# Kernel optimization log

Measured on AMD Instinct MI355X. Metric: run time of the kernel, lower is better.

The kernel has to match this reference:

```python
import jax, jax.numpy as jnp
import numpy as np

N_NODES = 50000
N_EDGES = 800000


def gcn_layer(x, edge_index, W, b):
    """PyG-style GCNConv: add self-loops, symmetric deg^-1/2 normalization,
    linear transform, scatter-sum aggregation at target nodes, plus bias."""
    n = x.shape[0]
    loops = jnp.arange(n)
    src = jnp.concatenate([edge_index[0], loops])  # [E+N]
    dst = jnp.concatenate([edge_index[1], loops])  # [E+N]
    deg = jax.ops.segment_sum(jnp.ones(src.shape, dtype=x.dtype), dst, num_segments=n)
    dinv = jnp.where(deg > 0, jax.lax.rsqrt(deg), jnp.zeros((), x.dtype))
    norm = dinv[src] * dinv[dst]               # [E+N]
    h = x @ W                                   # [N, out]
    msg = norm[:, None] * h[src]                # [E+N, out] gather
    out = jax.ops.segment_sum(msg, dst, num_segments=n)  # scatter-add
    return out + b


def setup_inputs() -> dict:
    key = jax.random.key(0)
    ks = jax.random.split(key, 8)
    features = jax.random.normal(ks[0], (N_NODES, 64), dtype=jnp.float32)
    edge_index1 = jax.random.randint(ks[1], (2, N_EDGES), 0, N_NODES)
    edge_index3 = jax.random.randint(ks[2], (2, N_EDGES), 0, N_NODES)
    edge_index9 = jax.random.randint(ks[3], (2, N_EDGES), 0, N_NODES)

    def glorot(k, fi, fo):
        lim = float(np.sqrt(6.0 / (fi + fo)))
        return jax.random.uniform(k, (fi, fo), minval=-lim, maxval=lim, dtype=jnp.float32)

    W1 = glorot(ks[4], 64, 64)
    W2 = glorot(ks[5], 64, 32)
    W3 = glorot(ks[6], 32, 16)
    b1 = jnp.zeros((64,), jnp.float32)
    b2 = jnp.zeros((32,), jnp.float32)
    b3 = jnp.zeros((16,), jnp.float32)
    return dict(features=features, edge_index1=edge_index1, edge_index3=edge_index3,
                edge_index9=edge_index9, W1=W1, b1=b1, W2=W2, b2=b2, W3=W3, b3=b3)


def reference(features, edge_index1, edge_index3, edge_index9, W1, b1, W2, b2, W3, b3):
    x = jax.nn.relu(gcn_layer(features, edge_index1, W1, b1))  # hop 1
    x = jax.nn.relu(gcn_layer(x, edge_index3, W2, b2))         # hop 3
    x = jax.nn.relu(gcn_layer(x, edge_index9, W3, b3))         # hop 9
    return x
```

## Files before the change

kernel.cpp:

```cpp
#include <hip/hip_runtime.h>
#include <hip/hip_fp16.h>


#define NB   256
#define NL   3
#define TB   (NB * NL)
#define CAPE 6400
#define CAPE_E (CAPE + 8)
#define CH   8192
#define P1T  512
#define EPT  (CH / P1T)
#define P2T  512

__device__ __forceinline__ void decode_chunk(int g, int nc1, int nc2,
                                             const int* s1, const int* d1, int E1,
                                             const int* s2, const int* d2, int E2,
                                             const int* s3, const int* d3, int E3,
                                             const int** src, const int** dst, int* E, int* l,
                                             int* gout) {
    if (g < nc1)            { *src = s1; *dst = d1; *E = E1; *l = 0; }
    else if (g < nc1 + nc2) { *src = s2; *dst = d2; *E = E2; *l = 1; g -= nc1; }
    else                    { *src = s3; *dst = d3; *E = E3; *l = 2; g -= nc1 + nc2; }
    *gout = g;
}

__device__ __forceinline__ void fma4(float4& a, float s, const float4& w) {
    a.x += s * w.x; a.y += s * w.y; a.z += s * w.z; a.w += s * w.w;
}
__device__ __forceinline__ void add4(float4& a, const float4& v) {
    a.x += v.x; a.y += v.y; a.z += v.z; a.w += v.w;
}
__device__ __forceinline__ float4 ldh4(const __half* h, size_t idx4) {
    uint2 r = ((const uint2*)h)[idx4];
    __half2 a = *reinterpret_cast<__half2*>(&r.x);
    __half2 b = *reinterpret_cast<__half2*>(&r.y);
    float2 fa = __half22float2(a), fb = __half22float2(b);
    return make_float4(fa.x, fa.y, fb.x, fb.y);
}
__device__ __forceinline__ void sth4(__half* h, size_t idx4, float4 v) {
    __half2 a = __floats2half2_rn(v.x, v.y);
    __half2 b = __floats2half2_rn(v.z, v.w);
    uint2 r;
    r.x = *reinterpret_cast<unsigned*>(&a);
    r.y = *reinterpret_cast<unsigned*>(&b);
    ((uint2*)h)[idx4] = r;
}

__global__ void __launch_bounds__(P1T) phase1(
        const int* __restrict__ s1, const int* __restrict__ d1, int E1,
        const int* __restrict__ s2, const int* __restrict__ d2, int E2,
        const int* __restrict__ s3, const int* __restrict__ d3, int E3,
        int nc1, int nc2, int W,
        int* __restrict__ gcur, unsigned int* __restrict__ pairBuf) {
    __shared__ int hist[TB];
    __shared__ int bo[TB];
    __shared__ int lcur[TB];
    for (int i = threadIdx.x; i < TB; i += P1T) hist[i] = 0;
    __syncthreads();
    const int* src; const int* dst; int E, l, g;
    decode_chunk(blockIdx.x, nc1, nc2, s1, d1, E1, s2, d2, E2, s3, d3, E3,
                 &src, &dst, &E, &l, &g);
    const int e0 = g * CH;
    const int lbase = l * NB;
    unsigned pv[EPT];
    int bn[EPT];
    if (E - e0 >= CH) {
        const int4* s4 = (const int4*)(src + e0);
        const int4* d4 = (const int4*)(dst + e0);
#pragma unroll
        for (int w = 0; w < EPT / 4; ++w) {
            int4 sv = s4[threadIdx.x + w * P1T];
            int4 dv = d4[threadIdx.x + w * P1T];
            int q, i = w * 4;
            q = dv.x / W; bn[i+0] = lbase + q; pv[i+0] = ((unsigned)sv.x << 9) | (unsigned)(dv.x - q * W);
            q = dv.y / W; bn[i+1] = lbase + q; pv[i+1] = ((unsigned)sv.y << 9) | (unsigned)(dv.y - q * W);
            q = dv.z / W; bn[i+2] = lbase + q; pv[i+2] = ((unsigned)sv.z << 9) | (unsigned)(dv.z - q * W);
            q = dv.w / W; bn[i+3] = lbase + q; pv[i+3] = ((unsigned)sv.w << 9) | (unsigned)(dv.w - q * W);
        }
    } else {
#pragma unroll
        for (int i = 0; i < EPT; ++i) {
            int e = e0 + threadIdx.x + i * P1T;
            if (e < E) {
                int s = src[e], d = dst[e];
                int q = d / W;
                bn[i] = lbase + q;
                pv[i] = ((unsigned)s << 9) | (unsigned)(d - q * W);
            } else bn[i] = -1;
        }
    }
#pragma unroll
    for (int i = 0; i < EPT; ++i)
        if (bn[i] >= 0) atomicAdd(&hist[bn[i]], 1);
    __syncthreads();
    for (int i = threadIdx.x; i < TB; i += P1T) {
        int c = hist[i];
        bo[i] = i * CAPE + (c ? atomicAdd(&gcur[i], c) : 0);
        lcur[i] = 0;
    }
    __syncthreads();
#pragma unroll
    for (int i = 0; i < EPT; ++i) {
        if (bn[i] >= 0) {
            int r = atomicAdd(&lcur[bn[i]], 1);
            int pos = bo[bn[i]] + r;
            if (pos < (bn[i] + 1) * CAPE) pairBuf[pos] = pv[i];
        }
    }
}

__global__ void __launch_bounds__(P2T) k2_phase2_gemm1(
        const unsigned int* __restrict__ pairBuf, const int* __restrict__ gcur,
        int n, int W,
        int* __restrict__ row_ptr, int* __restrict__ cnt_g,
        float* __restrict__ dinv, unsigned short* __restrict__ eidx,
        const float* __restrict__ x0, const float* __restrict__ W1g,
        __half* __restrict__ h1) {
    __shared__ __align__(16) char smem[17408];
    if (blockIdx.x < (unsigned)TB) {
        int* lcnt  = (int*)smem;
        int* lscan = lcnt + P2T;
        unsigned short* stage = (unsigned short*)(lscan + P2T);
        const int bid = blockIdx.x;
        const int l = bid / NB, k = bid % NB;
        const int lo = k * W;
        const int hi = min(n, lo + W);
        const int Wn = hi - lo;
        const int segE = min(gcur[bid], CAPE);
        const size_t base  = (size_t)bid * CAPE;
        const int    baseE = bid * CAPE_E;
        const int t = threadIdx.x;
        lcnt[t] = 0;
        __syncthreads();
        for (int i = t; i < segE; i += P2T)
            atomicAdd(&lcnt[pairBuf[base + i] & 511u], 1);
        __syncthreads();
        const int v = lcnt[t];
        const int vp = (v + 3) & ~3;
        lscan[t] = vp;
        __syncthreads();
        for (int off = 1; off < P2T; off <<= 1) {
            int add = (t >= off) ? lscan[t - off] : 0;
            __syncthreads();
            lscan[t] += add;
            __syncthreads();
        }
        const int pexcl = lscan[t] - vp;
        const int segEp = lscan[P2T - 1];
        if (t < Wn) {
            int node = l * n + lo + t;
            row_ptr[node] = baseE + pexcl;
            cnt_g[node] = v;
            dinv[node] = rsqrtf((float)v + 1.0f);
        }
        __syncthreads();
        lcnt[t] = pexcl;
        __syncthreads();
        const bool lds_ok = (segEp <= CAPE);
        for (int i = t; i < segE; i += P2T) {
            unsigned p = pairBuf[base + i];
            int pos = atomicAdd(&lcnt[p & 511u], 1);
            unsigned short s = (unsigned short)(p >> 9);
            if (lds_ok) stage[pos] = s;
            else if (pos < CAPE_E) eidx[baseE + pos] = s;
        }
        __syncthreads();
        if (lds_ok) {
            const int4* st4 = (const int4*)stage;
            int4* e4 = (int4*)(eidx + baseE);
            int m16 = (segEp + 7) >> 3;
            for (int i = t; i < m16; i += P2T) e4[i] = st4[i];
        }
    } else {
        float* Ws = (float*)smem;
        const int bid = blockIdx.x - TB;
        for (int i = threadIdx.x; i < 1024; i += P2T)
            ((float4*)Ws)[i] = ((const float4*)W1g)[i];
        __syncthreads();
        const int tc = threadIdx.x % 16;
        const int tr = threadIdx.x / 16;
        const int row0 = bid * 128 + tr * 4;
        const float4* x4 = (const float4*)x0;
        const float4* Ws4 = (const float4*)Ws;
        float4 acc[4];
#pragma unroll
        for (int r = 0; r < 4; ++r) acc[r] = make_float4(0.f, 0.f, 0.f, 0.f);
        int rowc[4];
#pragma unroll
        for (int r = 0; r < 4; ++r) rowc[r] = min(row0 + r, n - 1);
        for (int k0 = 0; k0 < 64; k0 += 4) {
            float4 wv0 = Ws4[(k0 + 0) * 16 + tc];
            float4 wv1 = Ws4[(k0 + 1) * 16 + tc];
            float4 wv2 = Ws4[(k0 + 2) * 16 + tc];
            float4 wv3 = Ws4[(k0 + 3) * 16 + tc];
#pragma unroll
            for (int r = 0; r < 4; ++r) {
                float4 xv = x4[(size_t)rowc[r] * 16 + (k0 / 4)];
                fma4(acc[r], xv.x, wv0);
                fma4(acc[r], xv.y, wv1);
                fma4(acc[r], xv.z, wv2);
                fma4(acc[r], xv.w, wv3);
            }
        }
#pragma unroll
        for (int r = 0; r < 4; ++r) {
            int row = row0 + r;
            if (row < n) sth4(h1, (size_t)row * 16 + tc, acc[r]);
        }
    }
}

__global__ void __launch_bounds__(256) k3_gather1_gemm2(
        const int* __restrict__ row_ptr, const int* __restrict__ cnt,
        const unsigned short* __restrict__ eidx, const float* __restrict__ dinv1,
        const float* __restrict__ dinv2,
        const __half* __restrict__ h1, const float* __restrict__ b1,
        const float* __restrict__ W2g, __half* __restrict__ h2, int n) {
    __shared__ float xs[16 * 68];
    __shared__ float W2s[64 * 32];
    for (int i = threadIdx.x; i < 512; i += 256)
        ((float4*)W2s)[i] = ((const float4*)W2g)[i];
    const int ln = threadIdx.x >> 4;
    const int f4 = threadIdx.x & 15;
    const int node = blockIdx.x * 16 + ln;
    if (node < n) {
        const int beg = row_ptr[node];
        const int m = cnt[node];
        float4 a0 = make_float4(0.f, 0.f, 0.f, 0.f), a1 = a0, a2 = a0, a3 = a0;
        int j = 0;
        for (; j + 8 <= m; j += 8) {
            ushort4 e0 = *(const ushort4*)(eidx + beg + j);
            ushort4 e1 = *(const ushort4*)(eidx + beg + j + 4);
            float w0 = dinv1[e0.x], w1 = dinv1[e0.y], w2 = dinv1[e0.z], w3 = dinv1[e0.w];
            float w4 = dinv1[e1.x], w5 = dinv1[e1.y], w6 = dinv1[e1.z], w7 = dinv1[e1.w];
            float4 v0 = ldh4(h1, (size_t)e0.x * 16 + f4);
            float4 v1 = ldh4(h1, (size_t)e0.y * 16 + f4);
            float4 v2 = ldh4(h1, (size_t)e0.z * 16 + f4);
            float4 v3 = ldh4(h1, (size_t)e0.w * 16 + f4);
            float4 v4 = ldh4(h1, (size_t)e1.x * 16 + f4);
            float4 v5 = ldh4(h1, (size_t)e1.y * 16 + f4);
            float4 v6 = ldh4(h1, (size_t)e1.z * 16 + f4);
            float4 v7 = ldh4(h1, (size_t)e1.w * 16 + f4);
            fma4(a0, w0, v0); fma4(a1, w1, v1); fma4(a2, w2, v2); fma4(a3, w3, v3);
            fma4(a0, w4, v4); fma4(a1, w5, v5); fma4(a2, w6, v6); fma4(a3, w7, v7);
        }
        if (j + 4 <= m) {
            ushort4 e0 = *(const ushort4*)(eidx + beg + j);
            fma4(a0, dinv1[e0.x], ldh4(h1, (size_t)e0.x * 16 + f4));
            fma4(a1, dinv1[e0.y], ldh4(h1, (size_t)e0.y * 16 + f4));
            fma4(a2, dinv1[e0.z], ldh4(h1, (size_t)e0.z * 16 + f4));
            fma4(a3, dinv1[e0.w], ldh4(h1, (size_t)e0.w * 16 + f4));
            j += 4;
        }
        for (; j < m; ++j) {
            int s = eidx[beg + j];
            fma4(a0, dinv1[s], ldh4(h1, (size_t)s * 16 + f4));
        }
        add4(a0, a1); add4(a2, a3); add4(a0, a2);
        float di = dinv1[node];
        float4 self = ldh4(h1, (size_t)node * 16 + f4);
        float4 bv = ((const float4*)b1)[f4];
        float4 o;
        o.x = di * (a0.x + di * self.x) + bv.x;
        o.y = di * (a0.y + di * self.y) + bv.y;
        o.z = di * (a0.z + di * self.z) + bv.z;
        o.w = di * (a0.w + di * self.w) + bv.w;
        o.x = o.x > 0.f ? o.x : 0.f;
        o.y = o.y > 0.f ? o.y : 0.f;
        o.z = o.z > 0.f ? o.z : 0.f;
        o.w = o.w > 0.f ? o.w : 0.f;
        *(float4*)&xs[ln * 68 + f4 * 4] = o;
    }
    __syncthreads();
    if (node < n) {
        const int c0 = f4 * 2;
        float s0 = 0.f, s1 = 0.f;
#pragma unroll
        for (int k = 0; k < 64; ++k) {
            float xv = xs[ln * 68 + k];
            s0 += xv * W2s[k * 32 + c0];
            s1 += xv * W2s[k * 32 + c0 + 1];
        }
        float d2 = dinv2[node];
        ((__half2*)h2)[(size_t)node * 16 + f4] = __floats2half2_rn(s0 * d2, s1 * d2);
    }
}

__global__ void __launch_bounds__(256) k4_gather2_gemm3(
        const int* __restrict__ row_ptr2, const int* __restrict__ cnt2,
        const unsigned short* __restrict__ eidx, const float* __restrict__ dinv2,
        const float* __restrict__ dinv3,
        const __half* __restrict__ h2, const float* __restrict__ b2,
        const float* __restrict__ W3g, __half* __restrict__ h3, int n) {
    __shared__ float xs[32 * 36];
    __shared__ float W3s[32 * 16];
    for (int i = threadIdx.x; i < 128; i += 256)
        ((float4*)W3s)[i] = ((const float4*)W3g)[i];
    const int ln = threadIdx.x >> 3;
    const int f4 = threadIdx.x & 7;
    const int node = blockIdx.x * 32 + ln;
    if (node < n) {
        const int beg = row_ptr2[node];
        const int m = cnt2[node];
        float4 a0 = make_float4(0.f, 0.f, 0.f, 0.f), a1 = a0, a2 = a0, a3 = a0;
        int j = 0;
        for (; j + 8 <= m; j += 8) {
            ushort4 e0 = *(const ushort4*)(eidx + beg + j);
            ushort4 e1 = *(const ushort4*)(eidx + beg + j + 4);
            add4(a0, ldh4(h2, (size_t)e0.x * 8 + f4));
            add4(a1, ldh4(h2, (size_t)e0.y * 8 + f4));
            add4(a2, ldh4(h2, (size_t)e0.z * 8 + f4));
            add4(a3, ldh4(h2, (size_t)e0.w * 8 + f4));
            add4(a0, ldh4(h2, (size_t)e1.x * 8 + f4));
            add4(a1, ldh4(h2, (size_t)e1.y * 8 + f4));
            add4(a2, ldh4(h2, (size_t)e1.z * 8 + f4));
            add4(a3, ldh4(h2, (size_t)e1.w * 8 + f4));
        }
        if (j + 4 <= m) {
            ushort4 e0 = *(const ushort4*)(eidx + beg + j);
            add4(a0, ldh4(h2, (size_t)e0.x * 8 + f4));
            add4(a1, ldh4(h2, (size_t)e0.y * 8 + f4));
            add4(a2, ldh4(h2, (size_t)e0.z * 8 + f4));
            add4(a3, ldh4(h2, (size_t)e0.w * 8 + f4));
            j += 4;
        }
        for (; j < m; ++j)
            add4(a0, ldh4(h2, (size_t)eidx[beg + j] * 8 + f4));
        add4(a0, a1); add4(a2, a3); add4(a0, a2);
        float di = dinv2[node];
        float4 self = ldh4(h2, (size_t)node * 8 + f4);
        float4 bv = ((const float4*)b2)[f4];
        float4 o;
        o.x = di * (a0.x + self.x) + bv.x;
        o.y = di * (a0.y + self.y) + bv.y;
        o.z = di * (a0.z + self.z) + bv.z;
        o.w = di * (a0.w + self.w) + bv.w;
        o.x = o.x > 0.f ? o.x : 0.f;
        o.y = o.y > 0.f ? o.y : 0.f;
        o.z = o.z > 0.f ? o.z : 0.f;
        o.w = o.w > 0.f ? o.w : 0.f;
        *(float4*)&xs[ln * 36 + f4 * 4] = o;
    }
    __syncthreads();
    if (node < n) {
        const int c0 = f4 * 2;
        float s0 = 0.f, s1 = 0.f;
#pragma unroll
        for (int k = 0; k < 32; ++k) {
            float xv = xs[ln * 36 + k];
            s0 += xv * W3s[k * 16 + c0];
            s1 += xv * W3s[k * 16 + c0 + 1];
        }
        float d3 = dinv3[node];
        ((__half2*)h3)[(size_t)node * 8 + f4] = __floats2half2_rn(s0 * d3, s1 * d3);
    }
}

__global__ void __launch_bounds__(256) k5_gather3(
        const int* __restrict__ row_ptr3, const int* __restrict__ cnt3,
        const unsigned short* __restrict__ eidx, const float* __restrict__ dinv3,
        const __half* __restrict__ h3, const float* __restrict__ b3,
        float* __restrict__ out, int n) {
    const int ln = threadIdx.x >> 2;
    const int f4 = threadIdx.x & 3;
    const int node = blockIdx.x * 64 + ln;
    if (node >= n) return;
    const int beg = row_ptr3[node];
    const int m = cnt3[node];
    float4 a0 = make_float4(0.f, 0.f, 0.f, 0.f), a1 = a0, a2 = a0, a3 = a0;
    int j = 0;
    for (; j + 8 <= m; j += 8) {
        ushort4 e0 = *(const ushort4*)(eidx + beg + j);
        ushort4 e1 = *(const ushort4*)(eidx + beg + j + 4);
        add4(a0, ldh4(h3, (size_t)e0.x * 4 + f4));
        add4(a1, ldh4(h3, (size_t)e0.y * 4 + f4));
        add4(a2, ldh4(h3, (size_t)e0.z * 4 + f4));
        add4(a3, ldh4(h3, (size_t)e0.w * 4 + f4));
        add4(a0, ldh4(h3, (size_t)e1.x * 4 + f4));
        add4(a1, ldh4(h3, (size_t)e1.y * 4 + f4));
        add4(a2, ldh4(h3, (size_t)e1.z * 4 + f4));
        add4(a3, ldh4(h3, (size_t)e1.w * 4 + f4));
    }
    if (j + 4 <= m) {
        ushort4 e0 = *(const ushort4*)(eidx + beg + j);
        add4(a0, ldh4(h3, (size_t)e0.x * 4 + f4));
        add4(a1, ldh4(h3, (size_t)e0.y * 4 + f4));
        add4(a2, ldh4(h3, (size_t)e0.z * 4 + f4));
        add4(a3, ldh4(h3, (size_t)e0.w * 4 + f4));
        j += 4;
    }
    for (; j < m; ++j)
        add4(a0, ldh4(h3, (size_t)eidx[beg + j] * 4 + f4));
    add4(a0, a1); add4(a2, a3); add4(a0, a2);
    float di = dinv3[node];
    float4 self = ldh4(h3, (size_t)node * 4 + f4);
    float4 bv = ((const float4*)b3)[f4];
    float4 o;
    o.x = di * (a0.x + self.x) + bv.x;
    o.y = di * (a0.y + self.y) + bv.y;
    o.z = di * (a0.z + self.z) + bv.z;
    o.w = di * (a0.w + self.w) + bv.w;
    o.x = o.x > 0.f ? o.x : 0.f;
    o.y = o.y > 0.f ? o.y : 0.f;
    o.z = o.z > 0.f ? o.z : 0.f;
    o.w = o.w > 0.f ? o.w : 0.f;
    ((float4*)out)[(size_t)node * 4 + f4] = o;
}

extern "C" void kernel_launch(void* const* d_in, const int* in_sizes, int n_in,
                              void* d_out, int out_size, void* d_ws, size_t ws_size,
                              hipStream_t stream) {
    const float* x0  = (const float*)d_in[0];
    const int*   ei1 = (const int*)d_in[1];
    const int*   ei3 = (const int*)d_in[2];
    const int*   ei9 = (const int*)d_in[3];
    const float* W1  = (const float*)d_in[4];
    const float* b1  = (const float*)d_in[5];
    const float* W2  = (const float*)d_in[6];
    const float* b2  = (const float*)d_in[7];
    const float* W3  = (const float*)d_in[8];
    const float* b3  = (const float*)d_in[9];

    const int n  = in_sizes[0] / 64;
    const int E1 = in_sizes[1] / 2;
    const int E3 = in_sizes[2] / 2;
    const int E9 = in_sizes[3] / 2;
    const int n3 = 3 * n;
    const int W  = (n + NB - 1) / NB;

    const int nc1 = (E1 + CH - 1) / CH;
    const int nc2 = (E3 + CH - 1) / CH;
    const int nc3 = (E9 + CH - 1) / CH;
    const int nchunks = nc1 + nc2 + nc3;
    const int gemmBlks = (n + 127) / 128;

    int* gcur    = (int*)d_ws;
    unsigned int* pairBuf = (unsigned int*)(gcur + TB);
    unsigned short* eidx = (unsigned short*)(pairBuf + (size_t)TB * CAPE);
    int* row_ptr = (int*)(eidx + (size_t)TB * CAPE_E);
    int* cnt     = row_ptr + n3;
    float* dinv  = (float*)(cnt + n3);
    __half* h1   = (__half*)(dinv + n3);
    __half* h2   = h1 + (size_t)n * 64;
    __half* h3   = h2 + (size_t)n * 32;

    hipMemsetAsync(gcur, 0, TB * sizeof(int), stream);
    phase1<<<nchunks, P1T, 0, stream>>>(ei1, ei1 + E1, E1, ei3, ei3 + E3, E3,
                                        ei9, ei9 + E9, E9, nc1, nc2, W, gcur, pairBuf);
    k2_phase2_gemm1<<<TB + gemmBlks, P2T, 0, stream>>>(
        pairBuf, gcur, n, W, row_ptr, cnt, dinv, eidx, x0, W1, h1);
    k3_gather1_gemm2<<<(n + 15) / 16, 256, 0, stream>>>(
        row_ptr, cnt, eidx, dinv, dinv + n, h1, b1, W2, h2, n);
    k4_gather2_gemm3<<<(n + 31) / 32, 256, 0, stream>>>(
        row_ptr + n, cnt + n, eidx, dinv + n, dinv + 2 * n, h2, b2, W3, h3, n);
    k5_gather3<<<(n + 63) / 64, 256, 0, stream>>>(
        row_ptr + 2 * n, cnt + 2 * n, eidx, dinv + 2 * n, h3, b3, (float*)d_out, n);
}
```

Before: 176.4 us.

## Stage phase1 bucket scatter in shared memory for coalesced pairBuf writes

Phase1 now sorts each chunk's edges by destination bucket in shared memory, using a block-wide prefix scan over the per-bucket histogram. It then writes pairBuf in bucket-contiguous order, so consecutive threads store to consecutive addresses instead of scattering randomly. The cost is an extra scan with several syncthreads and about 40KB of added LDS, which may lower occupancy. Histograms are also shrunk to one layer's worth of buckets.

```diff
diff --git a/kernel.cpp b/kernel.cpp
--- a/kernel.cpp
+++ b/kernel.cpp
@@ -52,10 +52,14 @@
         const int* __restrict__ s3, const int* __restrict__ d3, int E3,
         int nc1, int nc2, int W,
         int* __restrict__ gcur, unsigned int* __restrict__ pairBuf) {
-    __shared__ int hist[TB];
-    __shared__ int bo[TB];
-    __shared__ int lcur[TB];
-    for (int i = threadIdx.x; i < TB; i += P1T) hist[i] = 0;
+    __shared__ int hist[NB];
+    __shared__ int eofs[NB];
+    __shared__ int bo[NB];
+    __shared__ int lcur[NB];
+    __shared__ unsigned stage[CH];
+    __shared__ unsigned char stageQ[CH];
+    const int t = threadIdx.x;
+    for (int i = t; i < NB; i += P1T) hist[i] = 0;
     __syncthreads();
     const int* src; const int* dst; int E, l, g;
     decode_chunk(blockIdx.x, nc1, nc2, s1, d1, E1, s2, d2, E2, s3, d3, E3,
@@ -69,22 +73,22 @@
         const int4* d4 = (const int4*)(dst + e0);
 #pragma unroll
         for (int w = 0; w < EPT / 4; ++w) {
-            int4 sv = s4[threadIdx.x + w * P1T];
-            int4 dv = d4[threadIdx.x + w * P1T];
+            int4 sv = s4[t + w * P1T];
+            int4 dv = d4[t + w * P1T];
             int q, i = w * 4;
-            q = dv.x / W; bn[i+0] = lbase + q; pv[i+0] = ((unsigned)sv.x << 9) | (unsigned)(dv.x - q * W);
-            q = dv.y / W; bn[i+1] = lbase + q; pv[i+1] = ((unsigned)sv.y << 9) | (unsigned)(dv.y - q * W);
-            q = dv.z / W; bn[i+2] = lbase + q; pv[i+2] = ((unsigned)sv.z << 9) | (unsigned)(dv.z - q * W);
-            q = dv.w / W; bn[i+3] = lbase + q; pv[i+3] = ((unsigned)sv.w << 9) | (unsigned)(dv.w - q * W);
+            q = dv.x / W; bn[i+0] = q; pv[i+0] = ((unsigned)sv.x << 9) | (unsigned)(dv.x - q * W);
+            q = dv.y / W; bn[i+1] = q; pv[i+1] = ((unsigned)sv.y << 9) | (unsigned)(dv.y - q * W);
+            q = dv.z / W; bn[i+2] = q; pv[i+2] = ((unsigned)sv.z << 9) | (unsigned)(dv.z - q * W);
+            q = dv.w / W; bn[i+3] = q; pv[i+3] = ((unsigned)sv.w << 9) | (unsigned)(dv.w - q * W);
         }
     } else {
 #pragma unroll
         for (int i = 0; i < EPT; ++i) {
-            int e = e0 + threadIdx.x + i * P1T;
+            int e = e0 + t + i * P1T;
             if (e < E) {
                 int s = src[e], d = dst[e];
                 int q = d / W;
-                bn[i] = lbase + q;
+                bn[i] = q;
                 pv[i] = ((unsigned)s << 9) | (unsigned)(d - q * W);
             } else bn[i] = -1;
         }
@@ -93,19 +97,38 @@
     for (int i = 0; i < EPT; ++i)
         if (bn[i] >= 0) atomicAdd(&hist[bn[i]], 1);
     __syncthreads();
-    for (int i = threadIdx.x; i < TB; i += P1T) {
-        int c = hist[i];
-        bo[i] = i * CAPE + (c ? atomicAdd(&gcur[i], c) : 0);
-        lcur[i] = 0;
+    if (t < NB) eofs[t] = hist[t];
+    __syncthreads();
+    for (int off = 1; off < NB; off <<= 1) {
+        int add = (t < NB && t >= off) ? eofs[t - off] : 0;
+        __syncthreads();
+        if (t < NB) eofs[t] += add;
+        __syncthreads();
+    }
+    const int total = eofs[NB - 1];
+    int excl = 0;
+    if (t < NB) excl = eofs[t] - hist[t];
+    __syncthreads();
+    if (t < NB) {
+        eofs[t] = excl;
+        lcur[t] = excl;
+        int c = hist[t];
+        bo[t] = (lbase + t) * CAPE + (c ? atomicAdd(&gcur[lbase + t], c) : 0);
     }
     __syncthreads();
 #pragma unroll
     for (int i = 0; i < EPT; ++i) {
         if (bn[i] >= 0) {
             int r = atomicAdd(&lcur[bn[i]], 1);
-            int pos = bo[bn[i]] + r;
-            if (pos < (bn[i] + 1) * CAPE) pairBuf[pos] = pv[i];
-        }
+            stage[r] = pv[i];
+            stageQ[r] = (unsigned char)bn[i];
+        }
+    }
+    __syncthreads();
+    for (int i = t; i < total; i += P1T) {
+        int q = stageQ[i];
+        int k = bo[q] + (i - eofs[q]);
+        if (k < (lbase + q + 1) * CAPE) pairBuf[k] = stage[i];
     }
 }
 
```

Measured after the change: 167.4 us. -5.1%, faster.
